# Optimization experiments

Measured on AMD Instinct MI355X. Metric: run time of the kernel, lower is better.

Reference implementation:

```python
import jax, jax.numpy as jnp
import numpy as np

BN_EPS = 1e-5
MAX_NODES = 35  # sigmoid()*30+5 floored -> in [5, 34], strict bound 35


def _bn_eval(x, gamma, beta, rm, rv):
    # BatchNorm1d in eval mode with running statistics
    return (x - rm) * (gamma / jnp.sqrt(rv + BN_EPS)) + beta


def setup_inputs() -> dict:
    key = jax.random.key(0)
    ks = jax.random.split(key, 32)
    B, LD, E, ND = 131072, 32, 64, 11

    def lin(k, fan_in, fan_out):
        k1, k2 = jax.random.split(k)
        lim = 1.0 / np.sqrt(fan_in)
        w = jax.random.uniform(k1, (fan_in, fan_out), jnp.float32, -lim, lim)
        b = jax.random.uniform(k2, (fan_out,), jnp.float32, -lim, lim)
        return w, b

    lin_w, lin_b = lin(ks[0], LD + 1, E)
    nn1_w, nn1_b = lin(ks[1], E, E)
    nn2_w, nn2_b = lin(ks[2], E, 1)
    nd1_w, nd1_b = lin(ks[3], E, E)
    nd2_w, nd2_b = lin(ks[4], E, ND)
    pd1_w, pd1_b = lin(ks[5], E, E)
    pd2_w, pd2_b = lin(ks[6], E, 3)

    def bn_params(k):
        k1, k2, k3, k4 = jax.random.split(k, 4)
        gamma = 1.0 + 0.1 * jax.random.normal(k1, (E,), jnp.float32)
        beta = 0.1 * jax.random.normal(k2, (E,), jnp.float32)
        rm = 0.1 * jax.random.normal(k3, (E,), jnp.float32)
        rv = jax.random.uniform(k4, (E,), jnp.float32, 0.5, 1.5)
        return gamma, beta, rm, rv

    nd_gamma, nd_beta, nd_rm, nd_rv = bn_params(ks[7])
    pd_gamma, pd_beta, pd_rm, pd_rv = bn_params(ks[8])

    return dict(
        z=jax.random.normal(ks[9], (B, LD), jnp.float32),
        target_property=jax.random.normal(ks[10], (B,), jnp.float32),
        batch_size=B,
        lin_w=lin_w, lin_b=lin_b,
        nn1_w=nn1_w, nn1_b=nn1_b, nn2_w=nn2_w, nn2_b=nn2_b,
        nd1_w=nd1_w, nd1_b=nd1_b, nd_gamma=nd_gamma, nd_beta=nd_beta,
        nd_rm=nd_rm, nd_rv=nd_rv, nd2_w=nd2_w, nd2_b=nd2_b,
        pd1_w=pd1_w, pd1_b=pd1_b, pd_gamma=pd_gamma, pd_beta=pd_beta,
        pd_rm=pd_rm, pd_rv=pd_rv, pd2_w=pd2_w, pd2_b=pd2_b,
        node_scale=jnp.float32(4.5), node_shift=jnp.float32(4.5),
        pos_scale=jnp.float32(5.0), pos_shift=jnp.float32(0.0),
    )


def reference(z, target_property, batch_size,
              lin_w, lin_b,
              nn1_w, nn1_b, nn2_w, nn2_b,
              nd1_w, nd1_b, nd_gamma, nd_beta, nd_rm, nd_rv, nd2_w, nd2_b,
              pd1_w, pd1_b, pd_gamma, pd_beta, pd_rm, pd_rv, pd2_w, pd2_b,
              node_scale, node_shift, pos_scale, pos_shift):
    tp = target_property.reshape(-1, 1)
    h = jnp.concatenate([z, tp], axis=1) @ lin_w + lin_b  # [B, E]

    nn_logit = jax.nn.relu(h @ nn1_w + nn1_b) @ nn2_w + nn2_b  # [B, 1]
    num_nodes = (jax.nn.sigmoid(nn_logit) * 30.0 + 5.0).astype(jnp.int32)[:, 0]  # [B]

    # Expanded rows per graph are identical copies of h[i], so decode once per
    # graph (BN in eval mode) and repeat -> same math as per-graph expand+MLP.
    nf = _bn_eval(jax.nn.relu(h @ nd1_w + nd1_b), nd_gamma, nd_beta, nd_rm, nd_rv) @ nd2_w + nd2_b
    nf = nf * node_scale + node_shift  # [B, 11]
    pos = _bn_eval(jax.nn.relu(h @ pd1_w + pd1_b), pd_gamma, pd_beta, pd_rm, pd_rv) @ pd2_w + pd2_b
    pos = pos * pos_scale + pos_shift  # [B, 3]

    total = batch_size * MAX_NODES  # static padded bound on ragged concat length
    node_features = jnp.repeat(nf, num_nodes, axis=0, total_repeat_length=total)
    positions = jnp.repeat(pos, num_nodes, axis=0, total_repeat_length=total)
    return node_features, positions, num_nodes
```

## Files before the change

### kernel.cpp

```cpp
#include <hip/hip_runtime.h>
#include <math.h>

typedef unsigned int u32;
typedef unsigned short u16;
typedef __attribute__((ext_vector_type(8))) short short8v;
typedef __attribute__((ext_vector_type(4))) float f32x4;

#define NDF 11
#define MAXN 35
#define RS 72

__device__ __forceinline__ u16 f2bf(float x) {
    u32 b = __float_as_uint(x);
    u32 r = (b + 0x7fffu + ((b >> 16) & 1u)) >> 16;
    return (u16)r;
}
__device__ __forceinline__ float bf2f(u16 h) {
    return __uint_as_float(((u32)h) << 16);
}
__device__ __forceinline__ void splitbf(float x, u16& hi, u16& lo) {
    hi = f2bf(x);
    lo = f2bf(x - bf2f(hi));
}

__global__ void k_prep(const float* __restrict__ lin_w,
                       const float* __restrict__ nn1_w, const float* __restrict__ nn2_w,
                       const float* __restrict__ nd1_w, const float* __restrict__ nd2_w,
                       const float* __restrict__ pd1_w, const float* __restrict__ pd2_w,
                       const float* __restrict__ nd_g, const float* __restrict__ nd_be,
                       const float* __restrict__ nd_rm, const float* __restrict__ nd_rv,
                       const float* __restrict__ pd_g, const float* __restrict__ pd_be,
                       const float* __restrict__ pd_rm, const float* __restrict__ pd_rv,
                       u16* __restrict__ lint, u16* __restrict__ w1t3,
                       u16* __restrict__ w2t3, float* __restrict__ bnc)
{
    const int t0 = blockIdx.x * 256 + threadIdx.x;
    if (t0 < 64) {
        const float sc = nd_g[t0] / sqrtf(nd_rv[t0] + 1e-5f);
        bnc[t0]       = sc;
        bnc[64 + t0]  = nd_be[t0] - nd_rm[t0] * sc;
        const float sp = pd_g[t0] / sqrtf(pd_rv[t0] + 1e-5f);
        bnc[128 + t0] = sp;
        bnc[192 + t0] = pd_be[t0] - pd_rm[t0] * sp;
    }
    for (int i = t0; i < 64*RS; i += 4096) {
        const int n = i / RS, k = i % RS;
        const float v = (k < 33) ? lin_w[k*64 + n] : 0.f;
        u16 h, l; splitbf(v, h, l);
        lint[i] = h; lint[64*RS + i] = l;
    }
    for (int b = 0; b < 3; b++) {
        const float* M = (b == 0) ? nn1_w : (b == 1) ? nd1_w : pd1_w;
        u16* dst = w1t3 + (size_t)b * 2 * 64 * RS;
        for (int i = t0; i < 64*RS; i += 4096) {
            const int o = i / RS, k = i % RS;
            const float v = (k < 64) ? M[k*64 + o] : 0.f;
            u16 h, l; splitbf(v, h, l);
            dst[i] = h; dst[64*RS + i] = l;
        }
        u16* d2 = w2t3 + (size_t)b * 2 * 16 * RS;
        for (int i = t0; i < 16*RS; i += 4096) {
            const int n = i / RS, k = i % RS;
            float v = 0.f;
            if (k < 64) {
                if (b == 0)      { if (n == 14)           v = nn2_w[k]; }
                else if (b == 1) { if (n < 11)            v = nd2_w[k*11 + n]; }
                else             { if (n >= 11 && n < 14) v = pd2_w[k*3 + (n-11)]; }
            }
            u16 h, l; splitbf(v, h, l);
            d2[i] = h; d2[16*RS + i] = l;
        }
    }
}

__global__ __launch_bounds__(256)
void k_mfma(const float* __restrict__ z, const float* __restrict__ tpr,
            const float* __restrict__ lin_b,
            const u16* __restrict__ lint, const u16* __restrict__ w1t3,
            const u16* __restrict__ w2t3,
            const float* __restrict__ nn1_b, const float* __restrict__ nd1_b,
            const float* __restrict__ pd1_b,
            const float* __restrict__ nn2_b, const float* __restrict__ nd2_b,
            const float* __restrict__ pd2_b,
            const float* __restrict__ bnc,
            const float* __restrict__ nsc, const float* __restrict__ nsh,
            const float* __restrict__ psc, const float* __restrict__ psh,
            float* __restrict__ nf_g, float* __restrict__ pos_g,
            int* __restrict__ nn_int, float* __restrict__ out_nn,
            u32* __restrict__ fmask, int B)
{
    __shared__ __align__(16) u16 sXT[4][2*16*RS];
    __shared__ __align__(16) u16 sH[4][2*16*RS];

    const int t    = threadIdx.x;
    const int lane = t & 63;
    const int w    = t >> 6;
    u16* mX = sXT[w];
    u16* mH = sH[w];

    const int W = blockIdx.x * 4 + w;

    auto zeroXpad = [&]() {
        if (lane < 16) {
            #pragma unroll
            for (int pl = 0; pl < 2; pl++) {
                u16* base = mX + pl*16*RS;
                base[lane*RS + 33] = 0;
                u32* p = (u32*)(base + lane*RS + 34);
                #pragma unroll
                for (int q = 0; q < 15; q++) p[q] = 0;
            }
        }
    };

    auto gfrag = [&](const u16* base, int row0, int ks) -> short8v {
        const uint4 v = *(const uint4*)(base + (row0 + (lane & 15))*RS + ks*32 + ((lane >> 4) * 8));
        return __builtin_bit_cast(short8v, v);
    };
    short8v fLin[4][2], fW[3][4][2], fH2[3][2];
    #pragma unroll
    for (int nt = 0; nt < 4; nt++)
        #pragma unroll
        for (int ks = 0; ks < 2; ks++)
            fLin[nt][ks] = gfrag(lint, nt*16, ks);
    #pragma unroll
    for (int b = 0; b < 3; b++)
        #pragma unroll
        for (int nt = 0; nt < 4; nt++)
            #pragma unroll
            for (int ks = 0; ks < 2; ks++)
                fW[b][nt][ks] = gfrag(w1t3 + (size_t)b*2*64*RS, nt*16, ks);
    #pragma unroll
    for (int b = 0; b < 3; b++)
        #pragma unroll
        for (int ks = 0; ks < 2; ks++)
            fH2[b][ks] = gfrag(w2t3 + (size_t)b*2*16*RS, 0, ks);

    const int col = lane & 15;
    float bLin[4], bB1[3][4], bSc[2][4], bBi[2][4];
    #pragma unroll
    for (int nt = 0; nt < 4; nt++) {
        const int c = nt*16 + col;
        bLin[nt]    = lin_b[c];
        bB1[0][nt]  = nn1_b[c];
        bB1[1][nt]  = nd1_b[c];
        bB1[2][nt]  = pd1_b[c];
        bSc[0][nt]  = bnc[c];        bBi[0][nt] = bnc[64 + c];
        bSc[1][nt]  = bnc[128 + c];  bBi[1][nt] = bnc[192 + c];
    }
    const float epb = (col < 11) ? nd2_b[col] : (col < 14) ? pd2_b[col - 11] : 0.f;
    const float nn2b = nn2_b[0];
    const float a_ns = nsc[0], a_nh = nsh[0], a_ps = psc[0], a_ph = psh[0];

    auto ldfrag = [&](const u16* base, int ks) -> short8v {
        const uint4 v = *(const uint4*)(base + (lane & 15)*RS + ks*32 + ((lane >> 4) * 8));
        return __builtin_bit_cast(short8v, v);
    };

    u32 wavebits = 0;

    #pragma unroll 1
    for (int c = 0; c < 2; c++) {
        const int gb = (W*2 + c) * 16;
        if (gb >= B) break;

        zeroXpad();

        {
            const float4* zb = (const float4*)(z + (size_t)gb * 32);
            const float4 v0 = zb[(lane >> 2)*8 + (lane & 3)*2];
            const float4 v1 = zb[(lane >> 2)*8 + (lane & 3)*2 + 1];
            const float xv[8] = {v0.x, v0.y, v0.z, v0.w, v1.x, v1.y, v1.z, v1.w};
            u32 pkh[4], pkl[4];
            #pragma unroll
            for (int q = 0; q < 4; q++) {
                u16 h0, l0, h1, l1;
                splitbf(xv[2*q], h0, l0);
                splitbf(xv[2*q+1], h1, l1);
                pkh[q] = (u32)h0 | ((u32)h1 << 16);
                pkl[q] = (u32)l0 | ((u32)l1 << 16);
            }
            *(uint4*)(mX + (lane >> 2)*RS + (lane & 3)*8) = *(uint4*)pkh;
            *(uint4*)(mX + 16*RS + (lane >> 2)*RS + (lane & 3)*8) = *(uint4*)pkl;
            if (lane < 16) {
                u16 h, l; splitbf(tpr[gb + lane], h, l);
                mX[lane*RS + 32] = h;
                mX[16*RS + lane*RS + 32] = l;
            }
        }

        const short8v a0h = ldfrag(mX, 0);
        const short8v a1h = ldfrag(mX, 1);
        const short8v a0l = ldfrag(mX + 16*RS, 0);
        const short8v a1l = ldfrag(mX + 16*RS, 1);
        #pragma unroll
        for (int nt = 0; nt < 4; nt++) {
            const short8v bl0 = gfrag(lint + 64*RS, nt*16, 0);
            const short8v bl1 = gfrag(lint + 64*RS, nt*16, 1);
            f32x4 acc = {0.f, 0.f, 0.f, 0.f};
            acc = __builtin_amdgcn_mfma_f32_16x16x32_bf16(a0h, fLin[nt][0], acc, 0, 0, 0);
            acc = __builtin_amdgcn_mfma_f32_16x16x32_bf16(a1h, fLin[nt][1], acc, 0, 0, 0);
            acc = __builtin_amdgcn_mfma_f32_16x16x32_bf16(a0h, bl0, acc, 0, 0, 0);
            acc = __builtin_amdgcn_mfma_f32_16x16x32_bf16(a1h, bl1, acc, 0, 0, 0);
            acc = __builtin_amdgcn_mfma_f32_16x16x32_bf16(a0l, fLin[nt][0], acc, 0, 0, 0);
            acc = __builtin_amdgcn_mfma_f32_16x16x32_bf16(a1l, fLin[nt][1], acc, 0, 0, 0);
            const float bias = bLin[nt];
            #pragma unroll
            for (int r = 0; r < 4; r++) {
                const int row = (lane >> 4)*4 + r;
                u16 hh, hl; splitbf(acc[r] + bias, hh, hl);
                mH[row*RS + nt*16 + col] = hh;
                mH[16*RS + row*RS + nt*16 + col] = hl;
            }
        }

        u16* mT = mX;
        const short8v h0h = ldfrag(mH, 0);
        const short8v h1h = ldfrag(mH, 1);
        f32x4 acc2 = {0.f, 0.f, 0.f, 0.f};

        {
            const short8v h0l = ldfrag(mH + 16*RS, 0);
            const short8v h1l = ldfrag(mH + 16*RS, 1);
            const u16* wlo = w1t3 + 64*RS;
            #pragma unroll
            for (int nt = 0; nt < 4; nt++) {
                const short8v wl0 = gfrag(wlo, nt*16, 0);
                const short8v wl1 = gfrag(wlo, nt*16, 1);
                f32x4 acc = {0.f, 0.f, 0.f, 0.f};
                acc = __builtin_amdgcn_mfma_f32_16x16x32_bf16(h0h, fW[0][nt][0], acc, 0, 0, 0);
                acc = __builtin_amdgcn_mfma_f32_16x16x32_bf16(h1h, fW[0][nt][1], acc, 0, 0, 0);
                acc = __builtin_amdgcn_mfma_f32_16x16x32_bf16(h0h, wl0, acc, 0, 0, 0);
                acc = __builtin_amdgcn_mfma_f32_16x16x32_bf16(h1h, wl1, acc, 0, 0, 0);
                acc = __builtin_amdgcn_mfma_f32_16x16x32_bf16(h0l, fW[0][nt][0], acc, 0, 0, 0);
                acc = __builtin_amdgcn_mfma_f32_16x16x32_bf16(h1l, fW[0][nt][1], acc, 0, 0, 0);
                const float bb = bB1[0][nt];
                #pragma unroll
                for (int r = 0; r < 4; r++) {
                    const int row = (lane >> 4)*4 + r;
                    float rv = acc[r] + bb;
                    rv = rv > 0.f ? rv : 0.f;
                    u16 th, tl; splitbf(rv, th, tl);
                    mT[row*RS + nt*16 + col] = th;
                    mT[16*RS + row*RS + nt*16 + col] = tl;
                }
            }
            const short8v t0h = ldfrag(mT, 0);
            const short8v t1h = ldfrag(mT, 1);
            const short8v t0l = ldfrag(mT + 16*RS, 0);
            const short8v t1l = ldfrag(mT + 16*RS, 1);
            const short8v g2l0 = gfrag(w2t3 + 16*RS, 0, 0);
            const short8v g2l1 = gfrag(w2t3 + 16*RS, 0, 1);
            acc2 = __builtin_amdgcn_mfma_f32_16x16x32_bf16(t0h, fH2[0][0], acc2, 0, 0, 0);
            acc2 = __builtin_amdgcn_mfma_f32_16x16x32_bf16(t1h, fH2[0][1], acc2, 0, 0, 0);
            acc2 = __builtin_amdgcn_mfma_f32_16x16x32_bf16(t0h, g2l0, acc2, 0, 0, 0);
            acc2 = __builtin_amdgcn_mfma_f32_16x16x32_bf16(t1h, g2l1, acc2, 0, 0, 0);
            acc2 = __builtin_amdgcn_mfma_f32_16x16x32_bf16(t0l, fH2[0][0], acc2, 0, 0, 0);
            acc2 = __builtin_amdgcn_mfma_f32_16x16x32_bf16(t1l, fH2[0][1], acc2, 0, 0, 0);
        }

        #pragma unroll
        for (int b = 1; b < 3; b++) {
            #pragma unroll
            for (int nt = 0; nt < 4; nt++) {
                f32x4 acc = {0.f, 0.f, 0.f, 0.f};
                acc = __builtin_amdgcn_mfma_f32_16x16x32_bf16(h0h, fW[b][nt][0], acc, 0, 0, 0);
                acc = __builtin_amdgcn_mfma_f32_16x16x32_bf16(h1h, fW[b][nt][1], acc, 0, 0, 0);
                const float bb = bB1[b][nt];
                const float sc = bSc[b-1][nt];
                const float bi = bBi[b-1][nt];
                #pragma unroll
                for (int r = 0; r < 4; r++) {
                    const int row = (lane >> 4)*4 + r;
                    float rv = acc[r] + bb;
                    rv = rv > 0.f ? rv : 0.f;
                    mT[row*RS + nt*16 + col] = f2bf(fmaf(rv, sc, bi));
                }
            }
            const short8v t0 = ldfrag(mT, 0);
            const short8v t1 = ldfrag(mT, 1);
            acc2 = __builtin_amdgcn_mfma_f32_16x16x32_bf16(t0, fH2[b][0], acc2, 0, 0, 0);
            acc2 = __builtin_amdgcn_mfma_f32_16x16x32_bf16(t1, fH2[b][1], acc2, 0, 0, 0);
        }

        u32 chunkbits = 0;
        #pragma unroll
        for (int r = 0; r < 4; r++) {
            const int g = gb + (lane >> 4)*4 + r;
            const float v = acc2[r];
            bool fl = false;
            if (col < 11) {
                nf_g[(size_t)g*NDF + col] = fmaf(v + epb, a_ns, a_nh);
            } else if (col < 14) {
                pos_g[(size_t)g*3 + (col - 11)] = fmaf(v + epb, a_ps, a_ph);
            } else if (col == 14) {
                const float logit = v + nn2b;
                const float arg = fmaf(1.f / (1.f + expf(-logit)), 30.f, 5.f);
                int n;
                if (arg < 5.03f) {
                    n = 5;
                } else if (arg >= 34.97f) {
                    if (logit >= 38.f)      n = 35;
                    else { n = 34; fl = (logit > 37.f); }
                } else {
                    n = (int)arg;
                    fl = fabsf(arg - rintf(arg)) < 0.03f;
                }
                nn_int[g] = n;
                out_nn[g] = (float)n;
            }
            const unsigned long long m = __ballot(fl);
            chunkbits |= (u32)(((m >> 14) & 1ull) << r)
                       | (u32)(((m >> 30) & 1ull) << (4 + r))
                       | (u32)(((m >> 46) & 1ull) << (8 + r))
                       | (u32)(((m >> 62) & 1ull) << (12 + r));
        }
        wavebits |= chunkbits << (16 * c);
    }

    if (lane == 0) fmask[W] = wavebits;
    (void)B;
}

__global__ __launch_bounds__(256)
void k_fix(const float* __restrict__ z, const float* __restrict__ tpr,
           const float* __restrict__ lin_w, const float* __restrict__ lin_b,
           const float* __restrict__ nn1_w, const float* __restrict__ nn1_b,
           const float* __restrict__ nn2_w, const float* __restrict__ nn2_b,
           const u32* __restrict__ fmask, int* __restrict__ nn_int,
           float* __restrict__ out_nn, int B)
{
    __shared__ __align__(16) double hb[4][64];
    const int lane = threadIdx.x & 63;
    const int w = threadIdx.x >> 6;
    const int W = (blockIdx.x * 256 + threadIdx.x) >> 6;
    u32 mask = fmask[W];
    const double b2 = (double)nn2_b[0];

    while (mask) {
        const int bpos = __ffs(mask) - 1;
        mask &= mask - 1;
        const int g = W * 32 + bpos;

        double h0 = (double)lin_b[lane], h1 = 0.0, h2 = 0.0, h3 = 0.0;
        for (int j = 0; j < 32; j += 4) {
            h0 = fma((double)z[(size_t)g*32 + j],     (double)lin_w[j*64 + lane],     h0);
            h1 = fma((double)z[(size_t)g*32 + j + 1], (double)lin_w[(j+1)*64 + lane], h1);
            h2 = fma((double)z[(size_t)g*32 + j + 2], (double)lin_w[(j+2)*64 + lane], h2);
            h3 = fma((double)z[(size_t)g*32 + j + 3], (double)lin_w[(j+3)*64 + lane], h3);
        }
        h0 = fma((double)tpr[g], (double)lin_w[32*64 + lane], h0);
        hb[w][lane] = (h0 + h1) + (h2 + h3);

        const double2* hp = (const double2*)hb[w];
        double a0 = (double)nn1_b[lane], a1 = 0.0, a2 = 0.0, a3 = 0.0;
        for (int m = 0; m < 16; m++) {
            const double2 p = hp[2*m];
            const double2 q = hp[2*m + 1];
            a0 = fma(p.x, (double)nn1_w[(4*m+0)*64 + lane], a0);
            a1 = fma(p.y, (double)nn1_w[(4*m+1)*64 + lane], a1);
            a2 = fma(q.x, (double)nn1_w[(4*m+2)*64 + lane], a2);
            a3 = fma(q.y, (double)nn1_w[(4*m+3)*64 + lane], a3);
        }
        const double a = (a0 + a1) + (a2 + a3);
        double v = (a > 0.0) ? a * (double)nn2_w[lane] : 0.0;
        for (int d = 32; d > 0; d >>= 1) v += __shfl_xor(v, d);
        const double logit = v + b2;

        if (lane == 0) {
            const double sg = 1.0 / (1.0 + exp(-logit));
            const int n = (int)(sg * 30.0 + 5.0);
            nn_int[g] = n;
            out_nn[g] = (float)n;
        }
    }
    (void)B;
}

__global__ __launch_bounds__(256)
void k_scan1(const int* __restrict__ a, int* __restrict__ part, int* __restrict__ bsum)
{
    const int t = threadIdx.x;
    const int lane = t & 63;
    const int wid = t >> 6;
    const int g = blockIdx.x * 256 + t;
    int v = a[g];
    #pragma unroll
    for (int d = 1; d < 64; d <<= 1) {
        const int u = __shfl_up(v, d);
        if (lane >= d) v += u;
    }
    __shared__ int ws[4];
    if (lane == 63) ws[wid] = v;
    __syncthreads();
    int add = 0;
    #pragma unroll
    for (int q = 0; q < 3; q++) if (q < wid) add += ws[q];
    v += add;
    part[g] = v;
    if (t == 255) bsum[blockIdx.x] = v;
}

__global__ void k_scan2(const int* __restrict__ bsum, int* __restrict__ boff, int nb)
{
    const int t = threadIdx.x;
    const int lane = t & 63;
    const int wid = t >> 6;
    const int orig = bsum[t];
    int v = orig;
    #pragma unroll
    for (int d = 1; d < 64; d <<= 1) {
        const int u = __shfl_up(v, d);
        if (lane >= d) v += u;
    }
    __shared__ int ws[8];
    if (lane == 63) ws[wid] = v;
    __syncthreads();
    int add = 0;
    #pragma unroll
    for (int q = 0; q < 7; q++) if (q < wid) add += ws[q];
    v += add;
    boff[t] = v - orig;
    if (t == nb - 1) boff[nb] = v;
}

__global__ __launch_bounds__(256)
void k_expand(const int* __restrict__ part, const int* __restrict__ boff,
              const float* __restrict__ nf_g, const float* __restrict__ pos_g,
              float* __restrict__ out, int B, int T, int nb)
{
    __shared__ __align__(16) float s_nf[512*NDF];
    __shared__ __align__(16) float s_ps[512*3];
    __shared__ int s_boff[513];
    const int t = threadIdx.x;
    for (int i = t; i <= nb; i += 256) s_boff[i] = boff[i];
    __syncthreads();

    const int r0 = blockIdx.x * 512 + 2*t;

    int blo = 0, bhi = nb - 1;
    while (blo < bhi) {
        const int m = (blo + bhi + 1) >> 1;
        if (s_boff[m] <= r0) blo = m; else bhi = m - 1;
    }
    const int bi = blo;
    const int lr = r0 - s_boff[bi];
    int lo = 0, hi2 = 256;
    while (lo < hi2) {
        const int m = (lo + hi2) >> 1;
        if (part[bi*256 + m] <= lr) lo = m + 1; else hi2 = m;
    }
    int i0 = bi*256 + lo;
    i0 = (i0 < B) ? i0 : B - 1;
    const int Ci0 = s_boff[i0 >> 8] + part[i0];
    const int i1 = ((r0 + 1) >= Ci0 && i0 < B - 1) ? i0 + 1 : i0;

    #pragma unroll
    for (int j = 0; j < NDF; j++) {
        s_nf[(2*t)*NDF + j]     = nf_g[(size_t)i0*NDF + j];
        s_nf[(2*t + 1)*NDF + j] = nf_g[(size_t)i1*NDF + j];
    }
    #pragma unroll
    for (int j = 0; j < 3; j++) {
        s_ps[(2*t)*3 + j]     = pos_g[(size_t)i0*3 + j];
        s_ps[(2*t + 1)*3 + j] = pos_g[(size_t)i1*3 + j];
    }
    __syncthreads();

    float4* onf = (float4*)(out + (size_t)blockIdx.x * 512 * NDF);
    const float4* snf = (const float4*)s_nf;
    #pragma unroll
    for (int q = 0; q < 6; q++) {
        const int idx = q*256 + t;
        if (idx < 512*NDF/4) onf[idx] = snf[idx];
    }
    float4* ops = (float4*)(out + (size_t)T*NDF + (size_t)blockIdx.x * 512 * 3);
    const float4* sps = (const float4*)s_ps;
    #pragma unroll
    for (int q = 0; q < 2; q++) {
        const int idx = q*256 + t;
        if (idx < 384) ops[idx] = sps[idx];
    }
}

extern "C" void kernel_launch(void* const* d_in, const int* in_sizes, int n_in,
                              void* d_out, int out_size, void* d_ws, size_t ws_size,
                              hipStream_t stream)
{
    const float* z     = (const float*)d_in[0];
    const float* tpr   = (const float*)d_in[1];
    const int    B     = in_sizes[1];
    const int    T     = B * MAXN;

    const float* lin_w = (const float*)d_in[3];
    const float* lin_b = (const float*)d_in[4];
    const float* nn1_w = (const float*)d_in[5];
    const float* nn1_b = (const float*)d_in[6];
    const float* nn2_w = (const float*)d_in[7];
    const float* nn2_b = (const float*)d_in[8];
    const float* nd1_w = (const float*)d_in[9];
    const float* nd1_b = (const float*)d_in[10];
    const float* nd_g  = (const float*)d_in[11];
    const float* nd_be = (const float*)d_in[12];
    const float* nd_rm = (const float*)d_in[13];
    const float* nd_rv = (const float*)d_in[14];
    const float* nd2_w = (const float*)d_in[15];
    const float* nd2_b = (const float*)d_in[16];
    const float* pd1_w = (const float*)d_in[17];
    const float* pd1_b = (const float*)d_in[18];
    const float* pd_g  = (const float*)d_in[19];
    const float* pd_be = (const float*)d_in[20];
    const float* pd_rm = (const float*)d_in[21];
    const float* pd_rv = (const float*)d_in[22];
    const float* pd2_w = (const float*)d_in[23];
    const float* pd2_b = (const float*)d_in[24];
    const float* nsc   = (const float*)d_in[25];
    const float* nsh   = (const float*)d_in[26];
    const float* psc   = (const float*)d_in[27];
    const float* psh   = (const float*)d_in[28];

    float* out = (float*)d_out;

    char* wsp = (char*)d_ws;
    size_t off = 0;
    auto take = [&](size_t bytes) { void* p = wsp + off; off = (off + bytes + 255) & ~(size_t)255; return p; };

    u16*   lint  = (u16*)take(2*64*RS*sizeof(u16));
    u16*   w1t3  = (u16*)take(3*2*64*RS*sizeof(u16));
    u16*   w2t3  = (u16*)take(3*2*16*RS*sizeof(u16));
    float* bnc   = (float*)take(256*sizeof(float));
    u32*   fmask = (u32*)take((size_t)(B/32)*sizeof(u32));
    float* nf_g  = (float*)take((size_t)B*NDF*sizeof(float));
    float* pos_g = (float*)take((size_t)B*3*sizeof(float));
    int*   nn_i  = (int*)take((size_t)B*sizeof(int));
    int*   part  = (int*)take((size_t)B*sizeof(int));
    int*   bsum  = (int*)take(4096*sizeof(int));
    int*   boff  = (int*)take(4096*sizeof(int));

    const int nb = B / 256;

    k_prep<<<16, 256, 0, stream>>>(lin_w, nn1_w, nn2_w, nd1_w, nd2_w, pd1_w, pd2_w,
                                   nd_g, nd_be, nd_rm, nd_rv,
                                   pd_g, pd_be, pd_rm, pd_rv,
                                   lint, w1t3, w2t3, bnc);

    k_mfma<<<B/128, 256, 0, stream>>>(z, tpr, lin_b, lint, w1t3, w2t3,
                                      nn1_b, nd1_b, pd1_b, nn2_b, nd2_b, pd2_b,
                                      bnc, nsc, nsh, psc, psh,
                                      nf_g, pos_g, nn_i, out + (size_t)T*14,
                                      fmask, B);

    k_fix<<<1024, 256, 0, stream>>>(z, tpr, lin_w, lin_b, nn1_w, nn1_b, nn2_w, nn2_b,
                                    fmask, nn_i, out + (size_t)T*14, B);

    k_scan1<<<nb, 256, 0, stream>>>(nn_i, part, bsum);
    k_scan2<<<1, nb, 0, stream>>>(bsum, boff, nb);

    k_expand<<<T/512, 256, 0, stream>>>(part, boff, nf_g, pos_g, out, B, T, nb);

    (void)n_in; (void)out_size; (void)ws_size;
}
```

Baseline: 148.6 us.

## Fuse fix and scan kernels, fold target property into epilogue, trim lin MFMAs

Merges the fallback fix kernel and the first-level scan into one kernel, and moves the second-level scan of block sums into every k_expand block, cutting two launches and a small global round trip. In the MFMA kernel the target-property column is no longer packed into the padded K dimension. It is added as an fp32 FMA in the epilogue, which halves the lin-layer MFMAs and removes the padding zeroing. The trade-off is redundant scan work in each expand block and slightly different rounding for the tp term.

Result: faster. 136.1 us (-8.4%).

```diff
diff --git a/kernel.cpp b/kernel.cpp
--- a/kernel.cpp
+++ b/kernel.cpp
@@ -3,6 +3,7 @@
 
 typedef unsigned int u32;
 typedef unsigned short u16;
+typedef unsigned long long u64;
 typedef __attribute__((ext_vector_type(8))) short short8v;
 typedef __attribute__((ext_vector_type(4))) float f32x4;
 
@@ -75,7 +76,7 @@
 
 __global__ __launch_bounds__(256)
 void k_mfma(const float* __restrict__ z, const float* __restrict__ tpr,
-            const float* __restrict__ lin_b,
+            const float* __restrict__ lin_w, const float* __restrict__ lin_b,
             const u16* __restrict__ lint, const u16* __restrict__ w1t3,
             const u16* __restrict__ w2t3,
             const float* __restrict__ nn1_b, const float* __restrict__ nd1_b,
@@ -100,29 +101,14 @@
 
     const int W = blockIdx.x * 4 + w;
 
-    auto zeroXpad = [&]() {
-        if (lane < 16) {
-            #pragma unroll
-            for (int pl = 0; pl < 2; pl++) {
-                u16* base = mX + pl*16*RS;
-                base[lane*RS + 33] = 0;
-                u32* p = (u32*)(base + lane*RS + 34);
-                #pragma unroll
-                for (int q = 0; q < 15; q++) p[q] = 0;
-            }
-        }
-    };
-
     auto gfrag = [&](const u16* base, int row0, int ks) -> short8v {
         const uint4 v = *(const uint4*)(base + (row0 + (lane & 15))*RS + ks*32 + ((lane >> 4) * 8));
         return __builtin_bit_cast(short8v, v);
     };
-    short8v fLin[4][2], fW[3][4][2], fH2[3][2];
+    short8v fLin[4], fW[3][4][2], fH2[3][2];
     #pragma unroll
     for (int nt = 0; nt < 4; nt++)
-        #pragma unroll
-        for (int ks = 0; ks < 2; ks++)
-            fLin[nt][ks] = gfrag(lint, nt*16, ks);
+        fLin[nt] = gfrag(lint, nt*16, 0);
     #pragma unroll
     for (int b = 0; b < 3; b++)
         #pragma unroll
@@ -137,11 +123,12 @@
             fH2[b][ks] = gfrag(w2t3 + (size_t)b*2*16*RS, 0, ks);
 
     const int col = lane & 15;
-    float bLin[4], bB1[3][4], bSc[2][4], bBi[2][4];
+    float bLin[4], lin32c[4], bB1[3][4], bSc[2][4], bBi[2][4];
     #pragma unroll
     for (int nt = 0; nt < 4; nt++) {
         const int c = nt*16 + col;
         bLin[nt]    = lin_b[c];
+        lin32c[nt]  = lin_w[32*64 + c];
         bB1[0][nt]  = nn1_b[c];
         bB1[1][nt]  = nd1_b[c];
         bB1[2][nt]  = pd1_b[c];
@@ -163,8 +150,6 @@
     for (int c = 0; c < 2; c++) {
         const int gb = (W*2 + c) * 16;
         if (gb >= B) break;
-
-        zeroXpad();
 
         {
             const float4* zb = (const float4*)(z + (size_t)gb * 32);
@@ -182,33 +167,27 @@
             }
             *(uint4*)(mX + (lane >> 2)*RS + (lane & 3)*8) = *(uint4*)pkh;
             *(uint4*)(mX + 16*RS + (lane >> 2)*RS + (lane & 3)*8) = *(uint4*)pkl;
-            if (lane < 16) {
-                u16 h, l; splitbf(tpr[gb + lane], h, l);
-                mX[lane*RS + 32] = h;
-                mX[16*RS + lane*RS + 32] = l;
-            }
-        }
+        }
+
+        const float4 tq = *(const float4*)(tpr + gb + (lane >> 4)*4);
+        const float tpf[4] = {tq.x, tq.y, tq.z, tq.w};
 
         const short8v a0h = ldfrag(mX, 0);
-        const short8v a1h = ldfrag(mX, 1);
         const short8v a0l = ldfrag(mX + 16*RS, 0);
-        const short8v a1l = ldfrag(mX + 16*RS, 1);
         #pragma unroll
         for (int nt = 0; nt < 4; nt++) {
             const short8v bl0 = gfrag(lint + 64*RS, nt*16, 0);
-            const short8v bl1 = gfrag(lint + 64*RS, nt*16, 1);
             f32x4 acc = {0.f, 0.f, 0.f, 0.f};
-            acc = __builtin_amdgcn_mfma_f32_16x16x32_bf16(a0h, fLin[nt][0], acc, 0, 0, 0);
-            acc = __builtin_amdgcn_mfma_f32_16x16x32_bf16(a1h, fLin[nt][1], acc, 0, 0, 0);
+            acc = __builtin_amdgcn_mfma_f32_16x16x32_bf16(a0h, fLin[nt], acc, 0, 0, 0);
             acc = __builtin_amdgcn_mfma_f32_16x16x32_bf16(a0h, bl0, acc, 0, 0, 0);
-            acc = __builtin_amdgcn_mfma_f32_16x16x32_bf16(a1h, bl1, acc, 0, 0, 0);
-            acc = __builtin_amdgcn_mfma_f32_16x16x32_bf16(a0l, fLin[nt][0], acc, 0, 0, 0);
-            acc = __builtin_amdgcn_mfma_f32_16x16x32_bf16(a1l, fLin[nt][1], acc, 0, 0, 0);
+            acc = __builtin_amdgcn_mfma_f32_16x16x32_bf16(a0l, fLin[nt], acc, 0, 0, 0);
             const float bias = bLin[nt];
+            const float l32 = lin32c[nt];
             #pragma unroll
             for (int r = 0; r < 4; r++) {
                 const int row = (lane >> 4)*4 + r;
-                u16 hh, hl; splitbf(acc[r] + bias, hh, hl);
+                const float hv = fmaf(tpf[r], l32, acc[r] + bias);
+                u16 hh, hl; splitbf(hv, hh, hl);
                 mH[row*RS + nt*16 + col] = hh;
                 mH[16*RS + row*RS + nt*16 + col] = hl;
             }
@@ -309,7 +288,7 @@
                 nn_int[g] = n;
                 out_nn[g] = (float)n;
             }
-            const unsigned long long m = __ballot(fl);
+            const u64 m = __ballot(fl);
             chunkbits |= (u32)(((m >> 14) & 1ull) << r)
                        | (u32)(((m >> 30) & 1ull) << (4 + r))
                        | (u32)(((m >> 46) & 1ull) << (8 + r))
@@ -323,117 +302,122 @@
 }
 
 __global__ __launch_bounds__(256)
-void k_fix(const float* __restrict__ z, const float* __restrict__ tpr,
-           const float* __restrict__ lin_w, const float* __restrict__ lin_b,
-           const float* __restrict__ nn1_w, const float* __restrict__ nn1_b,
-           const float* __restrict__ nn2_w, const float* __restrict__ nn2_b,
-           const u32* __restrict__ fmask, int* __restrict__ nn_int,
-           float* __restrict__ out_nn, int B)
+void k_fixscan(const float* __restrict__ z, const float* __restrict__ tpr,
+               const float* __restrict__ lin_w, const float* __restrict__ lin_b,
+               const float* __restrict__ nn1_w, const float* __restrict__ nn1_b,
+               const float* __restrict__ nn2_w, const float* __restrict__ nn2_b,
+               const u32* __restrict__ fmask, int* __restrict__ nn_int,
+               float* __restrict__ out_nn,
+               int* __restrict__ part, int* __restrict__ bsum)
 {
     __shared__ __align__(16) double hb[4][64];
-    const int lane = threadIdx.x & 63;
-    const int w = threadIdx.x >> 6;
-    const int W = (blockIdx.x * 256 + threadIdx.x) >> 6;
-    u32 mask = fmask[W];
-    const double b2 = (double)nn2_b[0];
-
-    while (mask) {
-        const int bpos = __ffs(mask) - 1;
-        mask &= mask - 1;
-        const int g = W * 32 + bpos;
-
-        double h0 = (double)lin_b[lane], h1 = 0.0, h2 = 0.0, h3 = 0.0;
-        for (int j = 0; j < 32; j += 4) {
-            h0 = fma((double)z[(size_t)g*32 + j],     (double)lin_w[j*64 + lane],     h0);
-            h1 = fma((double)z[(size_t)g*32 + j + 1], (double)lin_w[(j+1)*64 + lane], h1);
-            h2 = fma((double)z[(size_t)g*32 + j + 2], (double)lin_w[(j+2)*64 + lane], h2);
-            h3 = fma((double)z[(size_t)g*32 + j + 3], (double)lin_w[(j+3)*64 + lane], h3);
-        }
-        h0 = fma((double)tpr[g], (double)lin_w[32*64 + lane], h0);
-        hb[w][lane] = (h0 + h1) + (h2 + h3);
-
-        const double2* hp = (const double2*)hb[w];
-        double a0 = (double)nn1_b[lane], a1 = 0.0, a2 = 0.0, a3 = 0.0;
-        for (int m = 0; m < 16; m++) {
-            const double2 p = hp[2*m];
-            const double2 q = hp[2*m + 1];
-            a0 = fma(p.x, (double)nn1_w[(4*m+0)*64 + lane], a0);
-            a1 = fma(p.y, (double)nn1_w[(4*m+1)*64 + lane], a1);
-            a2 = fma(q.x, (double)nn1_w[(4*m+2)*64 + lane], a2);
-            a3 = fma(q.y, (double)nn1_w[(4*m+3)*64 + lane], a3);
-        }
-        const double a = (a0 + a1) + (a2 + a3);
-        double v = (a > 0.0) ? a * (double)nn2_w[lane] : 0.0;
-        for (int d = 32; d > 0; d >>= 1) v += __shfl_xor(v, d);
-        const double logit = v + b2;
-
-        if (lane == 0) {
-            const double sg = 1.0 / (1.0 + exp(-logit));
-            const int n = (int)(sg * 30.0 + 5.0);
-            nn_int[g] = n;
-            out_nn[g] = (float)n;
-        }
-    }
-    (void)B;
-}
-
-__global__ __launch_bounds__(256)
-void k_scan1(const int* __restrict__ a, int* __restrict__ part, int* __restrict__ bsum)
-{
+    __shared__ int s_n[256];
+    __shared__ int ws[4];
+
     const int t = threadIdx.x;
     const int lane = t & 63;
-    const int wid = t >> 6;
-    const int g = blockIdx.x * 256 + t;
-    int v = a[g];
+    const int w = t >> 6;
+    const int g0 = blockIdx.x * 256;
+
+    s_n[t] = nn_int[g0 + t];
+
+    {
+        const u32 m0 = fmask[blockIdx.x*8 + w*2];
+        const u32 m1 = fmask[blockIdx.x*8 + w*2 + 1];
+        u64 mask = (u64)m0 | ((u64)m1 << 32);
+        const double b2 = (double)nn2_b[0];
+
+        while (mask) {
+            const int bpos = __ffsll(mask) - 1;
+            mask &= mask - 1;
+            const int g = g0 + w*64 + bpos;
+
+            double h0 = (double)lin_b[lane], h1 = 0.0, h2 = 0.0, h3 = 0.0;
+            for (int j = 0; j < 32; j += 4) {
+                h0 = fma((double)z[(size_t)g*32 + j],     (double)lin_w[j*64 + lane],     h0);
+                h1 = fma((double)z[(size_t)g*32 + j + 1], (double)lin_w[(j+1)*64 + lane], h1);
+                h2 = fma((double)z[(size_t)g*32 + j + 2], (double)lin_w[(j+2)*64 + lane], h2);
+                h3 = fma((double)z[(size_t)g*32 + j + 3], (double)lin_w[(j+3)*64 + lane], h3);
+            }
+            h0 = fma((double)tpr[g], (double)lin_w[32*64 + lane], h0);
+            hb[w][lane] = (h0 + h1) + (h2 + h3);
+
+            const double2* hp = (const double2*)hb[w];
+            double a0 = (double)nn1_b[lane], a1 = 0.0, a2 = 0.0, a3 = 0.0;
+            for (int m = 0; m < 16; m++) {
+                const double2 p = hp[2*m];
+                const double2 q = hp[2*m + 1];
+                a0 = fma(p.x, (double)nn1_w[(4*m+0)*64 + lane], a0);
+                a1 = fma(p.y, (double)nn1_w[(4*m+1)*64 + lane], a1);
+                a2 = fma(q.x, (double)nn1_w[(4*m+2)*64 + lane], a2);
+                a3 = fma(q.y, (double)nn1_w[(4*m+3)*64 + lane], a3);
+            }
+            const double a = (a0 + a1) + (a2 + a3);
+            double v = (a > 0.0) ? a * (double)nn2_w[lane] : 0.0;
+            for (int d = 32; d > 0; d >>= 1) v += __shfl_xor(v, d);
+            const double logit = v + b2;
+
+            if (lane == 0) {
+                const double sg = 1.0 / (1.0 + exp(-logit));
+                const int n = (int)(sg * 30.0 + 5.0);
+                s_n[w*64 + bpos] = n;
+                nn_int[g] = n;
+                out_nn[g] = (float)n;
+            }
+        }
+    }
+    __syncthreads();
+
+    int v = s_n[t];
     #pragma unroll
     for (int d = 1; d < 64; d <<= 1) {
         const int u = __shfl_up(v, d);
         if (lane >= d) v += u;
     }
-    __shared__ int ws[4];
-    if (lane == 63) ws[wid] = v;
+    if (lane == 63) ws[w] = v;
     __syncthreads();
     int add = 0;
     #pragma unroll
-    for (int q = 0; q < 3; q++) if (q < wid) add += ws[q];
+    for (int q = 0; q < 3; q++) if (q < w) add += ws[q];
     v += add;
-    part[g] = v;
+    part[g0 + t] = v;
     if (t == 255) bsum[blockIdx.x] = v;
 }
 
-__global__ void k_scan2(const int* __restrict__ bsum, int* __restrict__ boff, int nb)
-{
-    const int t = threadIdx.x;
-    const int lane = t & 63;
-    const int wid = t >> 6;
-    const int orig = bsum[t];
-    int v = orig;
-    #pragma unroll
-    for (int d = 1; d < 64; d <<= 1) {
-        const int u = __shfl_up(v, d);
-        if (lane >= d) v += u;
-    }
-    __shared__ int ws[8];
-    if (lane == 63) ws[wid] = v;
-    __syncthreads();
-    int add = 0;
-    #pragma unroll
-    for (int q = 0; q < 7; q++) if (q < wid) add += ws[q];
-    v += add;
-    boff[t] = v - orig;
-    if (t == nb - 1) boff[nb] = v;
-}
-
 __global__ __launch_bounds__(256)
-void k_expand(const int* __restrict__ part, const int* __restrict__ boff,
+void k_expand(const int* __restrict__ part, const int* __restrict__ bsum,
               const float* __restrict__ nf_g, const float* __restrict__ pos_g,
               float* __restrict__ out, int B, int T, int nb)
 {
     __shared__ __align__(16) float s_nf[512*NDF];
     __shared__ __align__(16) float s_ps[512*3];
     __shared__ int s_boff[513];
+    __shared__ int ws2[4];
     const int t = threadIdx.x;
-    for (int i = t; i <= nb; i += 256) s_boff[i] = boff[i];
+    const int lane = t & 63;
+    const int wid = t >> 6;
+
+    {
+        const int v0 = bsum[2*t];
+        const int v1 = bsum[2*t + 1];
+        const int s = v0 + v1;
+        int sc = s;
+        #pragma unroll
+        for (int d = 1; d < 64; d <<= 1) {
+            const int u = __shfl_up(sc, d);
+            if (lane >= d) sc += u;
+        }
+        if (lane == 63) ws2[wid] = sc;
+        __syncthreads();
+        int add = 0;
+        #pragma unroll
+        for (int q = 0; q < 3; q++) if (q < wid) add += ws2[q];
+        sc += add;
+        const int exc = sc - s;
+        s_boff[2*t]     = exc;
+        s_boff[2*t + 1] = exc + v0;
+        if (t == 255) s_boff[512] = sc;
+    }
     __syncthreads();
 
     const int r0 = blockIdx.x * 512 + 2*t;
@@ -535,7 +519,6 @@
     int*   nn_i  = (int*)take((size_t)B*sizeof(int));
     int*   part  = (int*)take((size_t)B*sizeof(int));
     int*   bsum  = (int*)take(4096*sizeof(int));
-    int*   boff  = (int*)take(4096*sizeof(int));
 
     const int nb = B / 256;
 
@@ -544,19 +527,17 @@
                                    pd_g, pd_be, pd_rm, pd_rv,
                                    lint, w1t3, w2t3, bnc);
 
-    k_mfma<<<B/128, 256, 0, stream>>>(z, tpr, lin_b, lint, w1t3, w2t3,
+    k_mfma<<<B/128, 256, 0, stream>>>(z, tpr, lin_w, lin_b, lint, w1t3, w2t3,
                                       nn1_b, nd1_b, pd1_b, nn2_b, nd2_b, pd2_b,
                                       bnc, nsc, nsh, psc, psh,
                                       nf_g, pos_g, nn_i, out + (size_t)T*14,
                                       fmask, B);
 
-    k_fix<<<1024, 256, 0, stream>>>(z, tpr, lin_w, lin_b, nn1_w, nn1_b, nn2_w, nn2_b,
-                                    fmask, nn_i, out + (size_t)T*14, B);
-
-    k_scan1<<<nb, 256, 0, stream>>>(nn_i, part, bsum);
-    k_scan2<<<1, nb, 0, stream>>>(bsum, boff, nb);
-
-    k_expand<<<T/512, 256, 0, stream>>>(part, boff, nf_g, pos_g, out, B, T, nb);
+    k_fixscan<<<nb, 256, 0, stream>>>(z, tpr, lin_w, lin_b, nn1_w, nn1_b,
+                                      nn2_w, nn2_b, fmask, nn_i,
+                                      out + (size_t)T*14, part, bsum);
+
+    k_expand<<<T/512, 256, 0, stream>>>(part, bsum, nf_g, pos_g, out, B, T, nb);
 
     (void)n_in; (void)out_size; (void)ws_size;
 }
```
